# Kernel tuning notes

Hardware: AMD Instinct MI355X
Metric: run time of the kernel (lower is better)

Reference implementation:

```python
import jax, jax.numpy as jnp
import numpy as np

PS = 2      # patch_size
TOPK = 3    # topk


def setup_inputs() -> dict:
    key = jax.random.key(0)
    x = jax.random.normal(key, (8, 128, 64, 64), dtype=jnp.float32)
    alpha = jnp.asarray(5.0, dtype=jnp.float32)  # nn.Parameter alpha
    return {"x": x, "alpha": alpha}


def _forward(x, alpha):
    ps = PS
    b, c, h, w = x.shape
    nph, npw = h // ps, w // ps
    npatch = nph * npw
    pa = ps * ps
    # F.normalize(p=2, dim=-3) with torch eps=1e-12
    norm = jnp.maximum(jnp.sqrt(jnp.sum(x * x, axis=1, keepdims=True)), 1e-12)
    x = x / norm
    # patchify -> [b, c, npatch, patch_area] (patches h-major, pixels row-major)
    xp = x.reshape(b, c, nph, ps, npw, ps).transpose(0, 1, 2, 4, 3, 5)
    xp = xp.reshape(b, c, npatch, pa)
    diag_idx = jnp.arange(ps) * (ps + 1)  # [0, 3] for ps=2
    # gather diagonal pixels of each patch -> [b, ps, npatch, c]
    xd = xp[:, :, :, diag_idx].transpose(0, 3, 2, 1)
    # patch correlation matmul -> [b, ps, npatch, npatch]
    corr = jnp.einsum('bpnc,bpmc->bpnm', xd, xd)
    avg = jnp.mean(corr, axis=1, keepdims=True)
    s = jnp.concatenate([corr, avg], axis=1)  # [b, ps+1, npatch, npatch]
    # ZeroWindow gaussian mask (rat_s=0.05); channel index = patch center (r,c)
    sr, sc = 0.05 * nph, 0.05 * npw
    rr = jnp.arange(nph, dtype=jnp.float32)
    cc = jnp.arange(npw, dtype=jnp.float32)
    cent_r, cent_c = jnp.meshgrid(rr, cc, indexing='ij')
    cent_r = cent_r.reshape(npatch)
    cent_c = cent_c.reshape(npatch)
    gr = jnp.exp(-(rr[None, :] - cent_r[:, None]) ** 2 / (2.0 * sr * sr))  # [npatch, nph]
    gc = jnp.exp(-(cc[None, :] - cent_c[:, None]) ** 2 / (2.0 * sc * sc))  # [npatch, npw]
    mask = (1.0 - gr[:, :, None] * gc[:, None, :]).reshape(npatch, npatch)
    s = s * mask[None, None]
    a = s * alpha
    # double (row + col) softmax
    s = jax.nn.softmax(a, axis=-1) * jax.nn.softmax(a, axis=-2)
    # expand avg channel to all patch pixels, scatter diagonal channels back
    new_x = jnp.broadcast_to(s[:, -1:], (b, pa, npatch, npatch))
    new_x = new_x.at[:, diag_idx].set(s[:, :ps])
    # un-patchify second npatch axis to spatial [b, npatch, h, w]
    y = jnp.swapaxes(new_x, 1, 3)  # [b, npatch, npatch, pa]
    y = y.reshape(b, npatch, nph, npw, ps, ps).transpose(0, 1, 2, 4, 3, 5)
    y = y.reshape(b, npatch, h, w)
    # topk over the npatch axis (dim=-3)
    vals = jax.lax.top_k(jnp.moveaxis(y, 1, -1), TOPK)[0]  # [b, h, w, k]
    return jnp.moveaxis(vals, -1, 1)  # [b, k, h, w]


def reference(x, alpha):
    return _forward(x, alpha)
```

## Files before the change

kernel.cpp:

```cpp
#include <hip/hip_runtime.h>
#include <hip/hip_bf16.h>
#include <math.h>

#define NB 8
#define NC 128
#define NH 64
#define NW 64
#define NP 1024
#define TWO_SIG2 5.12f
#define LOG2E 1.44269504089f

static const size_t PSUM_OFF_B = 0;
static const size_t PBUF_OFF_B = (size_t)NB * 3 * 4 * NP * 4;
static const size_t XD_OFF_B   = PBUF_OFF_B + (size_t)NB * NP * 3 * 4 * 3 * 4;

typedef __bf16 bf16x8 __attribute__((ext_vector_type(8)));
typedef float f32x4 __attribute__((ext_vector_type(4)));

__device__ __forceinline__ int iabs_(int v) { return v < 0 ? -v : v; }

#define INSERT3(v, A, Bq, Cq)                          \
  {                                                    \
    const float _na = fmaxf(A, (v));                   \
    const float _nb = __builtin_amdgcn_fmed3f(A, Bq, (v)); \
    Cq = __builtin_amdgcn_fmed3f(Bq, Cq, (v));         \
    A = _na;                                           \
    Bq = _nb;                                          \
  }

#define MERGE3(a0, a1, a2, b0, b1, b2)       \
  {                                          \
    const float _x1 = fmaxf(a0, b0);         \
    const float _y1 = fminf(a0, b0);         \
    const float _x2 = fmaxf(a1, b1);         \
    const float _z  = fmaxf(a2, b2);         \
    a0 = _x1;                                \
    a1 = fmaxf(_y1, _x2);                    \
    a2 = fmaxf(fminf(_y1, _x2), _z);         \
  }

__global__ __launch_bounds__(256) void k1_norm(const float* __restrict__ x,
                                               __hip_bfloat16* __restrict__ xd) {
  __shared__ __align__(16) float tile[NC * 65];
  const int chunk = blockIdx.x;
  const int p = blockIdx.y;
  const int b = blockIdx.z;
  const int t = threadIdx.x;
  const int pix = t & 63;
  const int cw = t >> 6;
  const int nbase = chunk * 64;

  {
    const int n = nbase + pix;
    const int i = ((n >> 5) << 1) + p;
    const int jf = (n & 31);
    const float* xb = x + (size_t)b * NC * NH * NW + (size_t)i * NW;
    for (int cc = 0; cc < 32; ++cc) {
      const int c = (cc << 2) + cw;
      const float2 v2 = ((const float2*)(xb + (size_t)c * NH * NW))[jf];
      tile[c * 65 + pix] = (p == 0) ? v2.x : v2.y;
    }
  }
  __syncthreads();

  const int lane = t & 63;
  const int w = t >> 6;
  for (int pg = 0; pg < 16; ++pg) {
    const int pixel = (pg << 2) + w;
    const float v0 = tile[lane * 65 + pixel];
    const float v1 = tile[(lane + 64) * 65 + pixel];
    float ss = v0 * v0 + v1 * v1;
#pragma unroll
    for (int m = 32; m >= 1; m >>= 1) ss += __shfl_xor(ss, m, 64);
    const float inv = 1.0f / fmaxf(sqrtf(ss), 1e-12f);
    __hip_bfloat16* xr = xd + ((size_t)((b * 2 + p) * NP) + nbase + pixel) * NC;
    xr[lane] = __float2bfloat16(v0 * inv);
    xr[lane + 64] = __float2bfloat16(v1 * inv);
  }
}

__global__ __launch_bounds__(256) void k2_sums(const ushort* __restrict__ xd,
                                               const float* __restrict__ alpha_p,
                                               float* __restrict__ psum) {
  __shared__ __align__(16) __bf16 As[2][64 * 136];
  __shared__ __align__(16) __bf16 Bs[2][64 * 136];
  __shared__ float er[32];
  __shared__ float erA[32];
  const int t = threadIdx.x;
  const float K = (*alpha_p) * LOG2E;
  if (t < 32) {
    const float e = __expf(-(float)(t * t) / TWO_SIG2);
    er[t] = e;
    erA[t] = K * e;
  }

  const int cchunk = blockIdx.x;
  const int rowtile = blockIdx.y;
  const int b = blockIdx.z;
  const int i0 = rowtile << 6;
  const int jb = cchunk << 8;

#pragma unroll
  for (int pl = 0; pl < 2; ++pl) {
    const float4* ga = (const float4*)(xd + ((size_t)(b * 2 + pl) * NP + i0) * NC);
#pragma unroll
    for (int it = 0; it < 4; ++it) {
      const int f = (it << 8) + t;
      const int r = f >> 4, q = f & 15;
      *(float4*)(&As[pl][r * 136 + q * 8]) = ga[f];
    }
  }

  const int wave = t >> 6;
  const int lane = t & 63;
  const int lrow = lane & 15;
  const int kq = lane >> 4;

  float sums[3][4];
#pragma unroll
  for (int ch = 0; ch < 3; ++ch)
#pragma unroll
    for (int reg = 0; reg < 4; ++reg) sums[ch][reg] = 0.f;

  for (int sc = 0; sc < 4; ++sc) {
    const int j0 = jb + (sc << 6);
    __syncthreads();
#pragma unroll
    for (int pl = 0; pl < 2; ++pl) {
      const float4* gb = (const float4*)(xd + ((size_t)(b * 2 + pl) * NP + j0) * NC);
#pragma unroll
      for (int it = 0; it < 4; ++it) {
        const int f = (it << 8) + t;
        const int r = f >> 4, q = f & 15;
        *(float4*)(&Bs[pl][r * 136 + q * 8]) = gb[f];
      }
    }
    __syncthreads();

    f32x4 acc[2][4];
#pragma unroll
    for (int pl = 0; pl < 2; ++pl)
#pragma unroll
      for (int ct = 0; ct < 4; ++ct)
#pragma unroll
        for (int u = 0; u < 4; ++u) acc[pl][ct][u] = 0.f;

#pragma unroll
    for (int kc = 0; kc < 4; ++kc) {
      const int kk = kc * 32 + (kq << 3);
      const bf16x8 a0 = *(const bf16x8*)(&As[0][(wave * 16 + lrow) * 136 + kk]);
      const bf16x8 a1 = *(const bf16x8*)(&As[1][(wave * 16 + lrow) * 136 + kk]);
#pragma unroll
      for (int ct = 0; ct < 4; ++ct) {
        const bf16x8 b0 = *(const bf16x8*)(&Bs[0][(ct * 16 + lrow) * 136 + kk]);
        const bf16x8 b1 = *(const bf16x8*)(&Bs[1][(ct * 16 + lrow) * 136 + kk]);
        acc[0][ct] = __builtin_amdgcn_mfma_f32_16x16x32_bf16(a0, b0, acc[0][ct], 0, 0, 0);
        acc[1][ct] = __builtin_amdgcn_mfma_f32_16x16x32_bf16(a1, b1, acc[1][ct], 0, 0, 0);
      }
    }

#pragma unroll
    for (int ct = 0; ct < 4; ++ct) {
      const int m = j0 + ct * 16 + lrow;
      const int rm = m >> 5, cm = m & 31;
#pragma unroll
      for (int reg = 0; reg < 4; ++reg) {
        const int n = i0 + wave * 16 + kq * 4 + reg;
        const int rn = n >> 5, cn = n & 31;
        const float fm2 = fmaf(-erA[iabs_(rn - rm)], er[iabs_(cn - cm)], K);
        const float g0 = fm2 * acc[0][ct][reg];
        const float g1 = fm2 * acc[1][ct][reg];
        sums[0][reg] += exp2f(g0);
        sums[1][reg] += exp2f(g1);
        sums[2][reg] += exp2f(0.5f * (g0 + g1));
      }
    }
  }

#pragma unroll
  for (int off = 1; off < 16; off <<= 1)
#pragma unroll
    for (int ch = 0; ch < 3; ++ch)
#pragma unroll
      for (int reg = 0; reg < 4; ++reg)
        sums[ch][reg] += __shfl_xor(sums[ch][reg], off, 64);

  if (lrow == 0) {
#pragma unroll
    for (int ch = 0; ch < 3; ++ch)
#pragma unroll
      for (int reg = 0; reg < 4; ++reg) {
        const int n = i0 + wave * 16 + kq * 4 + reg;
        psum[(((size_t)b * 3 + ch) * 4 + cchunk) * NP + n] = sums[ch][reg];
      }
  }
}

__global__ __launch_bounds__(256) void k4_topk(const ushort* __restrict__ xd,
                                               const float* __restrict__ alpha_p,
                                               const float* __restrict__ psum,
                                               float* __restrict__ pbuf) {
  __shared__ __align__(16) __bf16 As[2][64 * 136];
  __shared__ __align__(16) __bf16 Bs[2][64 * 136];
  __shared__ float er[32];
  __shared__ float erA[32];
  __shared__ float rsr[3][64];
  __shared__ float rsc[3][256];
  const int t = threadIdx.x;
  const float K = (*alpha_p) * LOG2E;
  if (t < 32) {
    const float e = __expf(-(float)(t * t) / TWO_SIG2);
    er[t] = e;
    erA[t] = K * e;
  }

  const int cchunk = blockIdx.x;
  const int rowtile = blockIdx.y;
  const int b = blockIdx.z;
  const int i0 = rowtile << 6;
  const int jb = cchunk << 8;

  if (t < 192) {
    const int ch = t >> 6, r = t & 63;
    const float* pp = psum + ((size_t)b * 3 + ch) * 4 * NP + i0 + r;
    rsr[ch][r] = 1.0f / (pp[0] + pp[NP] + pp[2 * NP] + pp[3 * NP]);
  }
#pragma unroll
  for (int ch = 0; ch < 3; ++ch) {
    const float* pp = psum + ((size_t)b * 3 + ch) * 4 * NP + jb + t;
    rsc[ch][t] = 1.0f / (pp[0] + pp[NP] + pp[2 * NP] + pp[3 * NP]);
  }

#pragma unroll
  for (int pl = 0; pl < 2; ++pl) {
    const float4* ga = (const float4*)(xd + ((size_t)(b * 2 + pl) * NP + i0) * NC);
#pragma unroll
    for (int it = 0; it < 4; ++it) {
      const int f = (it << 8) + t;
      const int r = f >> 4, q = f & 15;
      *(float4*)(&As[pl][r * 136 + q * 8]) = ga[f];
    }
  }

  const int wave = t >> 6;
  const int lane = t & 63;
  const int lrow = lane & 15;
  const int kq = lane >> 4;

  float tA[3][4], tB[3][4], tC[3][4];
#pragma unroll
  for (int ch = 0; ch < 3; ++ch)
#pragma unroll
    for (int reg = 0; reg < 4; ++reg) { tA[ch][reg] = 0.f; tB[ch][reg] = 0.f; tC[ch][reg] = 0.f; }

  for (int sc = 0; sc < 4; ++sc) {
    const int j0 = jb + (sc << 6);
    __syncthreads();
#pragma unroll
    for (int pl = 0; pl < 2; ++pl) {
      const float4* gb = (const float4*)(xd + ((size_t)(b * 2 + pl) * NP + j0) * NC);
#pragma unroll
      for (int it = 0; it < 4; ++it) {
        const int f = (it << 8) + t;
        const int r = f >> 4, q = f & 15;
        *(float4*)(&Bs[pl][r * 136 + q * 8]) = gb[f];
      }
    }
    __syncthreads();

    f32x4 acc[2][4];
#pragma unroll
    for (int pl = 0; pl < 2; ++pl)
#pragma unroll
      for (int ct = 0; ct < 4; ++ct)
#pragma unroll
        for (int u = 0; u < 4; ++u) acc[pl][ct][u] = 0.f;

#pragma unroll
    for (int kc = 0; kc < 4; ++kc) {
      const int kk = kc * 32 + (kq << 3);
      const bf16x8 a0 = *(const bf16x8*)(&As[0][(wave * 16 + lrow) * 136 + kk]);
      const bf16x8 a1 = *(const bf16x8*)(&As[1][(wave * 16 + lrow) * 136 + kk]);
#pragma unroll
      for (int ct = 0; ct < 4; ++ct) {
        const bf16x8 b0 = *(const bf16x8*)(&Bs[0][(ct * 16 + lrow) * 136 + kk]);
        const bf16x8 b1 = *(const bf16x8*)(&Bs[1][(ct * 16 + lrow) * 136 + kk]);
        acc[0][ct] = __builtin_amdgcn_mfma_f32_16x16x32_bf16(a0, b0, acc[0][ct], 0, 0, 0);
        acc[1][ct] = __builtin_amdgcn_mfma_f32_16x16x32_bf16(a1, b1, acc[1][ct], 0, 0, 0);
      }
    }

#pragma unroll
    for (int ct = 0; ct < 4; ++ct) {
      const int mc = sc * 64 + ct * 16 + lrow;
      const int m = jb + mc;
      const int rm = m >> 5, cm = m & 31;
      const float im0 = rsc[0][mc], im1 = rsc[1][mc], im2 = rsc[2][mc];
#pragma unroll
      for (int reg = 0; reg < 4; ++reg) {
        const int nr = wave * 16 + kq * 4 + reg;
        const int n = i0 + nr;
        const int rn = n >> 5, cn = n & 31;
        const float fm2 = fmaf(-erA[iabs_(rn - rm)], er[iabs_(cn - cm)], K);
        const float g0 = fm2 * acc[0][ct][reg];
        const float g1 = fm2 * acc[1][ct][reg];
        const float e0 = exp2f(g0);
        const float e1 = exp2f(g1);
        const float q0 = e0 * e0 * im0;
        const float q1 = e1 * e1 * im1;
        const float q2 = e0 * e1 * im2;
        INSERT3(q0, tA[0][reg], tB[0][reg], tC[0][reg]);
        INSERT3(q1, tA[1][reg], tB[1][reg], tC[1][reg]);
        INSERT3(q2, tA[2][reg], tB[2][reg], tC[2][reg]);
      }
    }
  }

#pragma unroll
  for (int off = 1; off < 16; off <<= 1)
#pragma unroll
    for (int ch = 0; ch < 3; ++ch)
#pragma unroll
      for (int reg = 0; reg < 4; ++reg) {
        const float b0 = __shfl_xor(tA[ch][reg], off, 64);
        const float b1 = __shfl_xor(tB[ch][reg], off, 64);
        const float b2 = __shfl_xor(tC[ch][reg], off, 64);
        MERGE3(tA[ch][reg], tB[ch][reg], tC[ch][reg], b0, b1, b2);
      }

  if (lrow == 0) {
#pragma unroll
    for (int ch = 0; ch < 3; ++ch)
#pragma unroll
      for (int reg = 0; reg < 4; ++reg) {
        const int nr = wave * 16 + kq * 4 + reg;
        const int n = i0 + nr;
        const float irn = rsr[ch][nr];
        const size_t base = ((((size_t)b * NP + n) * 3 + ch) * 4 + cchunk) * 3;
        pbuf[base + 0] = tA[ch][reg] * irn;
        pbuf[base + 1] = tB[ch][reg] * irn;
        pbuf[base + 2] = tC[ch][reg] * irn;
      }
  }
}

__global__ __launch_bounds__(256) void k5_merge(const float* __restrict__ pbuf,
                                                float* __restrict__ out) {
  const int tau = blockIdx.x * 256 + threadIdx.x;
  const int b = tau >> 10;
  const int n = tau & (NP - 1);
  const int rn = n >> 5, cn = n & 31;

  float f0[3], f1[3], f2[3];
#pragma unroll
  for (int ch = 0; ch < 3; ++ch) {
    const size_t base = (((size_t)tau * 3 + ch) * 4) * 3;
    f0[ch] = pbuf[base + 0];
    f1[ch] = pbuf[base + 1];
    f2[ch] = pbuf[base + 2];
#pragma unroll
    for (int p = 1; p < 4; ++p) {
      const float b0 = pbuf[base + p * 3 + 0];
      const float b1 = pbuf[base + p * 3 + 1];
      const float b2 = pbuf[base + p * 3 + 2];
      MERGE3(f0[ch], f1[ch], f2[ch], b0, b1, b2);
    }
  }

  float* ob = out + (size_t)b * 3 * (NH * NW);
  const int i00 = ((rn << 1) * NW) + (cn << 1);
#pragma unroll
  for (int tt = 0; tt < 3; ++tt) {
    float* op = ob + (size_t)tt * (NH * NW);
    const float r0 = (tt == 0) ? f0[0] : (tt == 1) ? f1[0] : f2[0];
    const float r1 = (tt == 0) ? f0[1] : (tt == 1) ? f1[1] : f2[1];
    const float r2 = (tt == 0) ? f0[2] : (tt == 1) ? f1[2] : f2[2];
    op[i00] = r0;
    op[i00 + NW + 1] = r1;
    op[i00 + 1] = r2;
    op[i00 + NW] = r2;
  }
}

extern "C" void kernel_launch(void* const* d_in, const int* in_sizes, int n_in,
                              void* d_out, int out_size, void* d_ws, size_t ws_size,
                              hipStream_t stream) {
  const float* x = (const float*)d_in[0];
  const float* alpha = (const float*)d_in[1];
  float* out = (float*)d_out;
  char* ws = (char*)d_ws;

  float* psum = (float*)(ws + PSUM_OFF_B);
  float* pbuf = (float*)(ws + PBUF_OFF_B);
  __hip_bfloat16* xd = (__hip_bfloat16*)(ws + XD_OFF_B);

  k1_norm<<<dim3(16, 2, NB), 256, 0, stream>>>(x, xd);
  k2_sums<<<dim3(4, 16, NB), 256, 0, stream>>>((const ushort*)xd, alpha, psum);
  k4_topk<<<dim3(4, 16, NB), 256, 0, stream>>>((const ushort*)xd, alpha, psum, pbuf);
  k5_merge<<<dim3(32), 256, 0, stream>>>(pbuf, out);
}
```

Baseline: 110.7 us.

## Compute gaussian mask inline and do top-k selection in log domain

Replaces the shared-memory er/erA lookup tables with an inline exp2 of the squared patch distance. It also swaps the libm exp2f for the raw hardware exp2 builtin. In the top-k kernel, candidates are compared as log2-domain values (2*g plus the negative log of the column sum), so the per-element exp2 and multiplies drop out. exp2 is applied only to the final three survivors. This trades LDS table reads and per-element transcendental work for cheaper FMAs, at the cost of small precision differences from the approximate exp2 and log.

```diff
diff --git a/kernel.cpp b/kernel.cpp
--- a/kernel.cpp
+++ b/kernel.cpp
@@ -16,8 +16,6 @@
 
 typedef __bf16 bf16x8 __attribute__((ext_vector_type(8)));
 typedef float f32x4 __attribute__((ext_vector_type(4)));
-
-__device__ __forceinline__ int iabs_(int v) { return v < 0 ? -v : v; }
 
 #define INSERT3(v, A, Bq, Cq)                          \
   {                                                    \
@@ -84,15 +82,9 @@
                                                float* __restrict__ psum) {
   __shared__ __align__(16) __bf16 As[2][64 * 136];
   __shared__ __align__(16) __bf16 Bs[2][64 * 136];
-  __shared__ float er[32];
-  __shared__ float erA[32];
   const int t = threadIdx.x;
   const float K = (*alpha_p) * LOG2E;
-  if (t < 32) {
-    const float e = __expf(-(float)(t * t) / TWO_SIG2);
-    er[t] = e;
-    erA[t] = K * e;
-  }
+  const float Cm = -(LOG2E / TWO_SIG2);
 
   const int cchunk = blockIdx.x;
   const int rowtile = blockIdx.y;
@@ -116,6 +108,10 @@
   const int lrow = lane & 15;
   const int kq = lane >> 4;
 
+  const int n0 = i0 + wave * 16 + kq * 4;
+  const float rnf = (float)(n0 >> 5);
+  const float cn0 = (float)(n0 & 31);
+
   float sums[3][4];
 #pragma unroll
   for (int ch = 0; ch < 3; ++ch)
@@ -162,17 +158,21 @@
 #pragma unroll
     for (int ct = 0; ct < 4; ++ct) {
       const int m = j0 + ct * 16 + lrow;
-      const int rm = m >> 5, cm = m & 31;
+      const float rmf = (float)(m >> 5);
+      const float cmf = (float)(m & 31);
+      const float dr = rnf - rmf;
+      const float dr2 = dr * dr;
 #pragma unroll
       for (int reg = 0; reg < 4; ++reg) {
-        const int n = i0 + wave * 16 + kq * 4 + reg;
-        const int rn = n >> 5, cn = n & 31;
-        const float fm2 = fmaf(-erA[iabs_(rn - rm)], er[iabs_(cn - cm)], K);
+        const float dc = cn0 + (float)reg - cmf;
+        const float d2 = fmaf(dc, dc, dr2);
+        const float em = __builtin_amdgcn_exp2f(d2 * Cm);
+        const float fm2 = fmaf(-em, K, K);
         const float g0 = fm2 * acc[0][ct][reg];
         const float g1 = fm2 * acc[1][ct][reg];
-        sums[0][reg] += exp2f(g0);
-        sums[1][reg] += exp2f(g1);
-        sums[2][reg] += exp2f(0.5f * (g0 + g1));
+        sums[0][reg] += __builtin_amdgcn_exp2f(g0);
+        sums[1][reg] += __builtin_amdgcn_exp2f(g1);
+        sums[2][reg] += __builtin_amdgcn_exp2f(0.5f * (g0 + g1));
       }
     }
   }
@@ -202,17 +202,11 @@
                                                float* __restrict__ pbuf) {
   __shared__ __align__(16) __bf16 As[2][64 * 136];
   __shared__ __align__(16) __bf16 Bs[2][64 * 136];
-  __shared__ float er[32];
-  __shared__ float erA[32];
   __shared__ float rsr[3][64];
-  __shared__ float rsc[3][256];
+  __shared__ float nlc[3][256];
   const int t = threadIdx.x;
   const float K = (*alpha_p) * LOG2E;
-  if (t < 32) {
-    const float e = __expf(-(float)(t * t) / TWO_SIG2);
-    er[t] = e;
-    erA[t] = K * e;
-  }
+  const float Cm = -(LOG2E / TWO_SIG2);
 
   const int cchunk = blockIdx.x;
   const int rowtile = blockIdx.y;
@@ -228,7 +222,7 @@
 #pragma unroll
   for (int ch = 0; ch < 3; ++ch) {
     const float* pp = psum + ((size_t)b * 3 + ch) * 4 * NP + jb + t;
-    rsc[ch][t] = 1.0f / (pp[0] + pp[NP] + pp[2 * NP] + pp[3 * NP]);
+    nlc[ch][t] = -__builtin_amdgcn_logf(pp[0] + pp[NP] + pp[2 * NP] + pp[3 * NP]);
   }
 
 #pragma unroll
@@ -247,11 +241,17 @@
   const int lrow = lane & 15;
   const int kq = lane >> 4;
 
+  const int n0 = i0 + wave * 16 + kq * 4;
+  const float rnf = (float)(n0 >> 5);
+  const float cn0 = (float)(n0 & 31);
+
   float tA[3][4], tB[3][4], tC[3][4];
 #pragma unroll
   for (int ch = 0; ch < 3; ++ch)
 #pragma unroll
-    for (int reg = 0; reg < 4; ++reg) { tA[ch][reg] = 0.f; tB[ch][reg] = 0.f; tC[ch][reg] = 0.f; }
+    for (int reg = 0; reg < 4; ++reg) {
+      tA[ch][reg] = -3.0e38f; tB[ch][reg] = -3.0e38f; tC[ch][reg] = -3.0e38f;
+    }
 
   for (int sc = 0; sc < 4; ++sc) {
     const int j0 = jb + (sc << 6);
@@ -294,24 +294,28 @@
     for (int ct = 0; ct < 4; ++ct) {
       const int mc = sc * 64 + ct * 16 + lrow;
       const int m = jb + mc;
-      const int rm = m >> 5, cm = m & 31;
-      const float im0 = rsc[0][mc], im1 = rsc[1][mc], im2 = rsc[2][mc];
+      const float rmf = (float)(m >> 5);
+      const float cmf = (float)(m & 31);
+      const float dr = rnf - rmf;
+      const float dr2 = dr * dr;
+      const float nl0 = nlc[0][mc];
+      const float nl1 = nlc[1][mc];
+      const float nl2 = nlc[2][mc];
 #pragma unroll
       for (int reg = 0; reg < 4; ++reg) {
-        const int nr = wave * 16 + kq * 4 + reg;
-        const int n = i0 + nr;
-        const int rn = n >> 5, cn = n & 31;
-        const float fm2 = fmaf(-erA[iabs_(rn - rm)], er[iabs_(cn - cm)], K);
-        const float g0 = fm2 * acc[0][ct][reg];
-        const float g1 = fm2 * acc[1][ct][reg];
-        const float e0 = exp2f(g0);
-        const float e1 = exp2f(g1);
-        const float q0 = e0 * e0 * im0;
-        const float q1 = e1 * e1 * im1;
-        const float q2 = e0 * e1 * im2;
-        INSERT3(q0, tA[0][reg], tB[0][reg], tC[0][reg]);
-        INSERT3(q1, tA[1][reg], tB[1][reg], tC[1][reg]);
-        INSERT3(q2, tA[2][reg], tB[2][reg], tC[2][reg]);
+        const float dc = cn0 + (float)reg - cmf;
+        const float d2 = fmaf(dc, dc, dr2);
+        const float em = __builtin_amdgcn_exp2f(d2 * Cm);
+        const float fm2 = fmaf(-em, K, K);
+        const float f2 = fm2 + fm2;
+        const float a0 = acc[0][ct][reg];
+        const float a1 = acc[1][ct][reg];
+        const float t0 = fmaf(f2, a0, nl0);
+        const float t1 = fmaf(f2, a1, nl1);
+        const float t2 = fmaf(fm2, a0 + a1, nl2);
+        INSERT3(t0, tA[0][reg], tB[0][reg], tC[0][reg]);
+        INSERT3(t1, tA[1][reg], tB[1][reg], tC[1][reg]);
+        INSERT3(t2, tA[2][reg], tB[2][reg], tC[2][reg]);
       }
     }
   }
@@ -337,9 +341,9 @@
         const int n = i0 + nr;
         const float irn = rsr[ch][nr];
         const size_t base = ((((size_t)b * NP + n) * 3 + ch) * 4 + cchunk) * 3;
-        pbuf[base + 0] = tA[ch][reg] * irn;
-        pbuf[base + 1] = tB[ch][reg] * irn;
-        pbuf[base + 2] = tC[ch][reg] * irn;
+        pbuf[base + 0] = __builtin_amdgcn_exp2f(tA[ch][reg]) * irn;
+        pbuf[base + 1] = __builtin_amdgcn_exp2f(tB[ch][reg]) * irn;
+        pbuf[base + 2] = __builtin_amdgcn_exp2f(tC[ch][reg]) * irn;
       }
   }
 }
```

Measured after the change: 104.7 us. 5.4% less time.
